# Performance work log

Measured on AMD Instinct MI355X. Metric: run time of the kernel, lower is better.

## Reference

```python
import jax, jax.numpy as jnp
import numpy as np

T, B, V, D, H, C = 2048, 32, 50257, 512, 768, 10


def setup_inputs() -> dict:
    key = jax.random.key(0)
    ks = jax.random.split(key, 11)
    s = 0.02
    return {
        "x": jax.random.randint(ks[0], (T, B), 0, V),
        "embed_table": jax.random.normal(ks[1], (V, D), jnp.float32) * s,
        "W_x": jax.random.normal(ks[2], (H, D), jnp.float32) * s,
        "W_f": jax.random.normal(ks[3], (H, D), jnp.float32) * s,
        "b_f": jax.random.normal(ks[4], (H,), jnp.float32) * s,
        "W_r": jax.random.normal(ks[5], (H, D), jnp.float32) * s,
        "b_r": jax.random.normal(ks[6], (H,), jnp.float32) * s,
        "W_cx": jax.random.normal(ks[7], (H, D), jnp.float32) * s,
        "b_cx": jax.random.normal(ks[8], (H,), jnp.float32) * s,
        "W_out": jax.random.normal(ks[9], (C, H), jnp.float32) * s,
        "b_out": jax.random.normal(ks[10], (C,), jnp.float32) * s,
    }


def reference(x, embed_table, W_x, W_f, b_f, W_r, b_r, W_cx, b_cx, W_out, b_out):
    # Embedding lookup: [T, B, D]
    e = embed_table[x]
    # Precompute all gate projections for every timestep (batched GEMMs).
    xp = jnp.einsum("tbd,hd->tbh", e, W_x)                 # x_t projection
    f = jax.nn.sigmoid(jnp.einsum("tbd,hd->tbh", e, W_f) + b_f)   # forget gate
    r = jax.nn.sigmoid(jnp.einsum("tbd,hd->tbh", e, W_r) + b_r)   # reset gate
    cx = jnp.einsum("tbd,hd->tbh", e, W_cx) + b_cx                # highway path

    c0 = jnp.zeros((B, H), e.dtype)  # init_hidden: zeros

    def step(c, inp):
        f_t, xp_t, r_t, cx_t = inp
        c = f_t * c + (1.0 - f_t) * xp_t
        h = r_t * jnp.tanh(c) + (1.0 - r_t) * cx_t
        return c, h

    _, ht = jax.lax.scan(step, c0, (f, xp, r, cx))  # ht: [T, B, H]

    # tanh -> max-pool over time -> tanh -> classifier
    pooled = jnp.max(jnp.tanh(ht), axis=0)          # [B, H]
    pooled = jnp.tanh(pooled)
    logit = pooled @ W_out.T + b_out                # [B, C]
    return logit
```

## Files before the change

### kernel.cpp

```cpp
#include <hip/hip_runtime.h>
#include <hip/hip_bf16.h>
#include <cstdint>
#include <cstddef>

#define T_DIM 2048
#define B_DIM 32
#define D_DIM 512
#define H_DIM 768
#define C_DIM 10
#define K_DIM D_DIM
#define N_DIM (4 * H_DIM)

#define TC 1024
#define NCHUNK (T_DIM / TC)
#define MC (TC * B_DIM)

#define L_SEG 64
#define S_SEG (TC / L_SEG)
#define BH (B_DIM * H_DIM)

typedef __attribute__((ext_vector_type(8))) short short8;
typedef __attribute__((ext_vector_type(4))) float float4v;

__device__ inline unsigned short f2bf(float f) {
  unsigned int u = __builtin_bit_cast(unsigned int, f);
  unsigned int r = (u + 0x7FFFu + ((u >> 16) & 1u)) >> 16;
  return (unsigned short)r;
}
__device__ inline float bf2f(unsigned short s) {
  unsigned int u = ((unsigned int)s) << 16;
  return __builtin_bit_cast(float, u);
}
__device__ inline float fast_rcp(float x) { return __builtin_amdgcn_rcpf(x); }
__device__ inline float fast_exp2(float x) { return __builtin_amdgcn_exp2f(x); }
__device__ inline float sigmoid_f(float x) {
  float e = fast_exp2(-1.4426950408889634f * x);
  return fast_rcp(1.0f + e);
}
__device__ inline float tanh_f(float x) {
  float e = fast_exp2(2.885390081777927f * x);
  return 1.0f - 2.0f * fast_rcp(e + 1.0f);
}
__device__ inline void gld16(const unsigned short* g, unsigned short* l) {
  __builtin_amdgcn_global_load_lds(
      (const __attribute__((address_space(1))) void*)g,
      (__attribute__((address_space(3))) void*)l, 16, 0, 0);
}
__device__ inline unsigned int pack_bf16x2(float lo, float hi) {
  return ((unsigned int)f2bf(hi) << 16) | (unsigned int)f2bf(lo);
}

__global__ __launch_bounds__(256) void gather_embed_kernel(
    const int* __restrict__ x_c, const float* __restrict__ table,
    unsigned short* __restrict__ ebfc) {
  int idx = blockIdx.x * 256 + threadIdx.x;
  int m = idx >> 7;
  int k4 = (idx & 127) << 2;
  int row = x_c[m];
  float4 v = *(const float4*)(table + (size_t)row * D_DIM + k4);
  ushort4 o;
  o.x = f2bf(v.x); o.y = f2bf(v.y); o.z = f2bf(v.z); o.w = f2bf(v.w);
  *(ushort4*)(ebfc + (size_t)m * D_DIM + k4) = o;
}

__global__ __launch_bounds__(256) void convert_w_kernel(
    const float* __restrict__ Wx, const float* __restrict__ Wf,
    const float* __restrict__ Wr, const float* __restrict__ Wcx,
    unsigned short* __restrict__ wcat) {
  int idx = blockIdx.x * 256 + threadIdx.x;
  int n = idx >> 7;
  int k4 = (idx & 127) << 2;
  int mat = n / H_DIM;
  int h = n - mat * H_DIM;
  const float* src = (mat == 0) ? Wx : (mat == 1) ? Wf : (mat == 2) ? Wr : Wcx;
  float4 v = *(const float4*)(src + (size_t)h * D_DIM + k4);
  ushort4 o;
  o.x = f2bf(v.x); o.y = f2bf(v.y); o.z = f2bf(v.z); o.w = f2bf(v.w);
  *(ushort4*)(wcat + (size_t)n * D_DIM + k4) = o;
}

#define BM 128
#define BN 128
#define BK 32

__global__ __launch_bounds__(256) void gemm_kernel(
    const unsigned short* __restrict__ ebfc,
    const unsigned short* __restrict__ wcat,
    const float* __restrict__ b_f, const float* __restrict__ b_r,
    const float* __restrict__ b_cx,
    unsigned short* __restrict__ projc) {
  __shared__ __align__(16) unsigned short As[2][4096];
  __shared__ __align__(16) unsigned short Bs[2][4096];

  int tid  = threadIdx.x;
  int wave = tid >> 6;
  int lane = tid & 63;
  int quad = lane >> 4;
  int l16  = lane & 15;
  int m0 = blockIdx.y * BM;
  int n0 = blockIdx.x * BN;
  int wn = (wave & 1) * 64;
  int wm = (wave >> 1) * 64;

  int row0 = tid >> 2;
  int cl0  = (tid & 3) ^ ((row0 >> 1) & 3);
  int row1 = 64 + row0;
  int cl1  = (tid & 3) ^ ((row1 >> 1) & 3);

  const unsigned short* gA0 = ebfc + (size_t)(m0 + row0) * K_DIM + cl0 * 8;
  const unsigned short* gA1 = ebfc + (size_t)(m0 + row1) * K_DIM + cl1 * 8;
  const unsigned short* gB0 = wcat + (size_t)(n0 + row0) * K_DIM + cl0 * 8;
  const unsigned short* gB1 = wcat + (size_t)(n0 + row1) * K_DIM + cl1 * 8;

  float4v acc[4][4] = {};

#define STAGE(buf, kt) do { \
    gld16(gA0 + (kt), As[buf] + tid * 8); \
    gld16(gB0 + (kt), Bs[buf] + tid * 8); \
    gld16(gA1 + (kt), As[buf] + 2048 + tid * 8); \
    gld16(gB1 + (kt), Bs[buf] + 2048 + tid * 8); } while (0)

  STAGE(0, 0);
  __syncthreads();

#pragma unroll
  for (int ki = 0; ki < K_DIM / BK; ki++) {
    const int cur = ki & 1;
    if (ki + 1 < K_DIM / BK) STAGE(cur ^ 1, (ki + 1) * BK);
    short8 wf[4], ef[4];
#pragma unroll
    for (int i = 0; i < 4; i++) {
      int r = wn + i * 16 + l16;
      int p = quad ^ ((r >> 1) & 3);
      wf[i] = *(const short8*)(Bs[cur] + r * BK + p * 8);
    }
#pragma unroll
    for (int j = 0; j < 4; j++) {
      int r = wm + j * 16 + l16;
      int p = quad ^ ((r >> 1) & 3);
      ef[j] = *(const short8*)(As[cur] + r * BK + p * 8);
    }
#pragma unroll
    for (int i = 0; i < 4; i++)
#pragma unroll
      for (int j = 0; j < 4; j++)
        acc[i][j] = __builtin_amdgcn_mfma_f32_16x16x32_bf16(wf[i], ef[j], acc[i][j], 0, 0, 0);
    __syncthreads();
  }

  int mat = n0 / H_DIM;
  int hb = n0 - mat * H_DIM;
  size_t matBase = (size_t)mat * MC * H_DIM;
  const float* bias = (mat == 1) ? b_f : (mat == 2) ? b_r : b_cx;
#pragma unroll
  for (int i = 0; i < 4; i++) {
    int h0 = hb + wn + i * 16 + quad * 4;
    float4 bv;
    if (mat == 0) { bv.x = bv.y = bv.z = bv.w = 0.0f; }
    else          { bv = *(const float4*)(bias + h0); }
#pragma unroll
    for (int j = 0; j < 4; j++) {
      int m = m0 + wm + j * 16 + l16;
      float v0 = acc[i][j][0] + bv.x;
      float v1 = acc[i][j][1] + bv.y;
      float v2 = acc[i][j][2] + bv.z;
      float v3 = acc[i][j][3] + bv.w;
      if (mat == 1 || mat == 2) {
        v0 = sigmoid_f(v0); v1 = sigmoid_f(v1);
        v2 = sigmoid_f(v2); v3 = sigmoid_f(v3);
      }
      uint2 pk;
      pk.x = pack_bf16x2(v0, v1);
      pk.y = pack_bf16x2(v2, v3);
      *(uint2*)(projc + matBase + (size_t)m * H_DIM + h0) = pk;
    }
  }
}

__global__ __launch_bounds__(128) void scan1_kernel(
    const unsigned short* __restrict__ projc,
    float* __restrict__ Pw, float* __restrict__ Qw) {
  int blk = blockIdx.x;
  int seg = blk / (BH / 512);
  int q   = blk % (BH / 512);
  int e4  = (q * 128 + threadIdx.x) * 4;
  const size_t mstr = (size_t)MC * H_DIM;
  size_t idx0 = (size_t)(seg * L_SEG) * BH + e4;
  float p0 = 1.f, p1 = 1.f, p2 = 1.f, p3 = 1.f;
  float c0 = 0.f, c1 = 0.f, c2 = 0.f, c3 = 0.f;
#pragma unroll 4
  for (int t = 0; t < L_SEG; t++) {
    size_t id = idx0 + (size_t)t * BH;
    ushort4 xp = *(const ushort4*)(projc + id);
    ushort4 ff = *(const ushort4*)(projc + mstr + id);
    float f0 = bf2f(ff.x), f1 = bf2f(ff.y), f2 = bf2f(ff.z), f3 = bf2f(ff.w);
    c0 = fmaf(f0, c0 - bf2f(xp.x), bf2f(xp.x));
    c1 = fmaf(f1, c1 - bf2f(xp.y), bf2f(xp.y));
    c2 = fmaf(f2, c2 - bf2f(xp.z), bf2f(xp.z));
    c3 = fmaf(f3, c3 - bf2f(xp.w), bf2f(xp.w));
    p0 *= f0; p1 *= f1; p2 *= f2; p3 *= f3;
  }
  int o = seg * BH + e4;
  *(float4*)(Pw + o) = make_float4(p0, p1, p2, p3);
  *(float4*)(Qw + o) = make_float4(c0, c1, c2, c3);
}

__global__ __launch_bounds__(256) void prefix_kernel(
    const float* __restrict__ Pw, const float* __restrict__ Qw,
    float* __restrict__ cin, float* __restrict__ c_state,
    const float* __restrict__ segmax, float* __restrict__ hm_state,
    int first, int hm_init) {
  int gid = blockIdx.x * 256 + threadIdx.x;
  float c = first ? 0.f : c_state[gid];
#pragma unroll
  for (int s = 0; s < S_SEG; s++) {
    cin[s * BH + gid] = c;
    c = fmaf(Pw[s * BH + gid], c, Qw[s * BH + gid]);
  }
  c_state[gid] = c;
  if (!first) {
    float m = segmax[gid];
#pragma unroll
    for (int s = 1; s < S_SEG; s++) m = fmaxf(m, segmax[s * BH + gid]);
    hm_state[gid] = hm_init ? m : fmaxf(hm_state[gid], m);
  }
}

__global__ __launch_bounds__(128) void scan2_kernel(
    const unsigned short* __restrict__ projc,
    const float* __restrict__ cin, float* __restrict__ segmax) {
  int blk = blockIdx.x;
  int seg = blk / (BH / 512);
  int q   = blk % (BH / 512);
  int e4  = (q * 128 + threadIdx.x) * 4;
  const size_t mstr = (size_t)MC * H_DIM;
  size_t idx0 = (size_t)(seg * L_SEG) * BH + e4;
  int o = seg * BH + e4;
  float4 cv = *(const float4*)(cin + o);
  float c0 = cv.x, c1 = cv.y, c2 = cv.z, c3 = cv.w;
  float m0 = -1e30f, m1 = -1e30f, m2 = -1e30f, m3 = -1e30f;
#pragma unroll 2
  for (int t = 0; t < L_SEG; t++) {
    size_t id = idx0 + (size_t)t * BH;
    ushort4 xp = *(const ushort4*)(projc + id);
    ushort4 ff = *(const ushort4*)(projc + mstr + id);
    ushort4 rr = *(const ushort4*)(projc + 2 * mstr + id);
    ushort4 cx = *(const ushort4*)(projc + 3 * mstr + id);
    c0 = fmaf(bf2f(ff.x), c0 - bf2f(xp.x), bf2f(xp.x));
    c1 = fmaf(bf2f(ff.y), c1 - bf2f(xp.y), bf2f(xp.y));
    c2 = fmaf(bf2f(ff.z), c2 - bf2f(xp.z), bf2f(xp.z));
    c3 = fmaf(bf2f(ff.w), c3 - bf2f(xp.w), bf2f(xp.w));
    float h0 = fmaf(bf2f(rr.x), tanh_f(c0) - bf2f(cx.x), bf2f(cx.x));
    float h1 = fmaf(bf2f(rr.y), tanh_f(c1) - bf2f(cx.y), bf2f(cx.y));
    float h2 = fmaf(bf2f(rr.z), tanh_f(c2) - bf2f(cx.z), bf2f(cx.z));
    float h3 = fmaf(bf2f(rr.w), tanh_f(c3) - bf2f(cx.w), bf2f(cx.w));
    m0 = fmaxf(m0, h0); m1 = fmaxf(m1, h1);
    m2 = fmaxf(m2, h2); m3 = fmaxf(m3, h3);
  }
  *(float4*)(segmax + o) = make_float4(m0, m1, m2, m3);
}

__global__ __launch_bounds__(256) void pool_final_kernel(
    const float* __restrict__ segmax, const float* __restrict__ hm_state,
    float* __restrict__ pooled) {
  int gid = blockIdx.x * 256 + threadIdx.x;
  float m = hm_state[gid];
#pragma unroll
  for (int s = 0; s < S_SEG; s++) m = fmaxf(m, segmax[s * BH + gid]);
  pooled[gid] = tanh_f(tanh_f(m));
}

__global__ __launch_bounds__(64) void classifier_kernel(
    const float* __restrict__ pooled, const float* __restrict__ W_out,
    const float* __restrict__ b_out, float* __restrict__ out) {
  int b = blockIdx.x / C_DIM;
  int c = blockIdx.x % C_DIM;
  int lane = threadIdx.x;
  float s = 0.0f;
#pragma unroll
  for (int i = 0; i < H_DIM / 64; i++) {
    int h = i * 64 + lane;
    s += pooled[(size_t)b * H_DIM + h] * W_out[(size_t)c * H_DIM + h];
  }
#pragma unroll
  for (int off = 32; off; off >>= 1) s += __shfl_down(s, off, 64);
  if (lane == 0) out[b * C_DIM + c] = s + b_out[c];
}

extern "C" void kernel_launch(void* const* d_in, const int* in_sizes, int n_in,
                              void* d_out, int out_size, void* d_ws, size_t ws_size,
                              hipStream_t stream) {
  const int*   x     = (const int*)d_in[0];
  const float* table = (const float*)d_in[1];
  const float* W_x   = (const float*)d_in[2];
  const float* W_f   = (const float*)d_in[3];
  const float* b_f   = (const float*)d_in[4];
  const float* W_r   = (const float*)d_in[5];
  const float* b_r   = (const float*)d_in[6];
  const float* W_cx  = (const float*)d_in[7];
  const float* b_cx  = (const float*)d_in[8];
  const float* W_out = (const float*)d_in[9];
  const float* b_out = (const float*)d_in[10];

  char* ws = (char*)d_ws;
  size_t off = 0;
  unsigned short* wcat  = (unsigned short*)(ws + off); off += (size_t)N_DIM * K_DIM * 2;
  unsigned short* ebfc  = (unsigned short*)(ws + off); off += (size_t)MC * K_DIM * 2;
  unsigned short* projc = (unsigned short*)(ws + off); off += (size_t)4 * MC * H_DIM * 2;
  float* Pw     = (float*)(ws + off); off += (size_t)S_SEG * BH * 4;
  float* Qw     = (float*)(ws + off); off += (size_t)S_SEG * BH * 4;
  float* cin    = (float*)(ws + off); off += (size_t)S_SEG * BH * 4;
  float* segmax = (float*)(ws + off); off += (size_t)S_SEG * BH * 4;
  float* c_st   = (float*)(ws + off); off += (size_t)BH * 4;
  float* hm_st  = (float*)(ws + off); off += (size_t)BH * 4;
  float* pooled = (float*)(ws + off); off += (size_t)BH * 4;

  convert_w_kernel<<<(N_DIM * K_DIM / 4) / 256, 256, 0, stream>>>(W_x, W_f, W_r, W_cx, wcat);

  dim3 g(N_DIM / BN, MC / BM);
  for (int ch = 0; ch < NCHUNK; ch++) {
    gather_embed_kernel<<<(MC * K_DIM / 4) / 256, 256, 0, stream>>>(x + (size_t)ch * MC, table, ebfc);
    gemm_kernel<<<g, 256, 0, stream>>>(ebfc, wcat, b_f, b_r, b_cx, projc);
    scan1_kernel<<<S_SEG * (BH / 512), 128, 0, stream>>>(projc, Pw, Qw);
    prefix_kernel<<<BH / 256, 256, 0, stream>>>(Pw, Qw, cin, c_st, segmax, hm_st,
                                                ch == 0, ch == 1);
    scan2_kernel<<<S_SEG * (BH / 512), 128, 0, stream>>>(projc, cin, segmax);
  }
  pool_final_kernel<<<BH / 256, 256, 0, stream>>>(segmax, hm_st, pooled);
  classifier_kernel<<<B_DIM * C_DIM, 64, 0, stream>>>(pooled, W_out, b_out, (float*)d_out);
}
```

Measured before the change: 610.2 us.

## Load GEMM MFMA fragments directly from global memory into registers, drop LDS staging

The projection GEMM no longer stages A/B tiles through shared memory with global_load_lds and barriers. Each wave loads its own MFMA fragments straight from global memory into double-buffered registers, prefetching the next K slice. The launch bounds also request three blocks per CU. This removes the LDS traffic and the __syncthreads calls, but loses the sharing of tiles across waves, so each element is fetched from global/L2 twice as often, and the extra register buffers may add register pressure.

```diff
diff --git a/kernel.cpp b/kernel.cpp
--- a/kernel.cpp
+++ b/kernel.cpp
@@ -40,11 +40,6 @@
 __device__ inline float tanh_f(float x) {
   float e = fast_exp2(2.885390081777927f * x);
   return 1.0f - 2.0f * fast_rcp(e + 1.0f);
-}
-__device__ inline void gld16(const unsigned short* g, unsigned short* l) {
-  __builtin_amdgcn_global_load_lds(
-      (const __attribute__((address_space(1))) void*)g,
-      (__attribute__((address_space(3))) void*)l, 16, 0, 0);
 }
 __device__ inline unsigned int pack_bf16x2(float lo, float hi) {
   return ((unsigned int)f2bf(hi) << 16) | (unsigned int)f2bf(lo);
@@ -83,15 +78,12 @@
 #define BN 128
 #define BK 32
 
-__global__ __launch_bounds__(256) void gemm_kernel(
+__global__ __launch_bounds__(256, 3) void gemm_kernel(
     const unsigned short* __restrict__ ebfc,
     const unsigned short* __restrict__ wcat,
     const float* __restrict__ b_f, const float* __restrict__ b_r,
     const float* __restrict__ b_cx,
     unsigned short* __restrict__ projc) {
-  __shared__ __align__(16) unsigned short As[2][4096];
-  __shared__ __align__(16) unsigned short Bs[2][4096];
-
   int tid  = threadIdx.x;
   int wave = tid >> 6;
   int lane = tid & 63;
@@ -102,50 +94,39 @@
   int wn = (wave & 1) * 64;
   int wm = (wave >> 1) * 64;
 
-  int row0 = tid >> 2;
-  int cl0  = (tid & 3) ^ ((row0 >> 1) & 3);
-  int row1 = 64 + row0;
-  int cl1  = (tid & 3) ^ ((row1 >> 1) & 3);
-
-  const unsigned short* gA0 = ebfc + (size_t)(m0 + row0) * K_DIM + cl0 * 8;
-  const unsigned short* gA1 = ebfc + (size_t)(m0 + row1) * K_DIM + cl1 * 8;
-  const unsigned short* gB0 = wcat + (size_t)(n0 + row0) * K_DIM + cl0 * 8;
-  const unsigned short* gB1 = wcat + (size_t)(n0 + row1) * K_DIM + cl1 * 8;
+  const unsigned short* aw[4];
+  const unsigned short* ae[4];
+#pragma unroll
+  for (int i = 0; i < 4; i++)
+    aw[i] = wcat + (size_t)(n0 + wn + i * 16 + l16) * K_DIM + quad * 8;
+#pragma unroll
+  for (int j = 0; j < 4; j++)
+    ae[j] = ebfc + (size_t)(m0 + wm + j * 16 + l16) * K_DIM + quad * 8;
 
   float4v acc[4][4] = {};
-
-#define STAGE(buf, kt) do { \
-    gld16(gA0 + (kt), As[buf] + tid * 8); \
-    gld16(gB0 + (kt), Bs[buf] + tid * 8); \
-    gld16(gA1 + (kt), As[buf] + 2048 + tid * 8); \
-    gld16(gB1 + (kt), Bs[buf] + 2048 + tid * 8); } while (0)
-
-  STAGE(0, 0);
-  __syncthreads();
+  short8 wf[2][4], ef[2][4];
+#pragma unroll
+  for (int i = 0; i < 4; i++) {
+    wf[0][i] = *(const short8*)(aw[i]);
+    ef[0][i] = *(const short8*)(ae[i]);
+  }
 
 #pragma unroll
   for (int ki = 0; ki < K_DIM / BK; ki++) {
-    const int cur = ki & 1;
-    if (ki + 1 < K_DIM / BK) STAGE(cur ^ 1, (ki + 1) * BK);
-    short8 wf[4], ef[4];
-#pragma unroll
-    for (int i = 0; i < 4; i++) {
-      int r = wn + i * 16 + l16;
-      int p = quad ^ ((r >> 1) & 3);
-      wf[i] = *(const short8*)(Bs[cur] + r * BK + p * 8);
+    const int cur = ki & 1, nxt = cur ^ 1;
+    if (ki + 1 < K_DIM / BK) {
+      const int ko = (ki + 1) * BK;
+#pragma unroll
+      for (int i = 0; i < 4; i++) {
+        wf[nxt][i] = *(const short8*)(aw[i] + ko);
+        ef[nxt][i] = *(const short8*)(ae[i] + ko);
+      }
     }
 #pragma unroll
-    for (int j = 0; j < 4; j++) {
-      int r = wm + j * 16 + l16;
-      int p = quad ^ ((r >> 1) & 3);
-      ef[j] = *(const short8*)(As[cur] + r * BK + p * 8);
-    }
-#pragma unroll
     for (int i = 0; i < 4; i++)
 #pragma unroll
       for (int j = 0; j < 4; j++)
-        acc[i][j] = __builtin_amdgcn_mfma_f32_16x16x32_bf16(wf[i], ef[j], acc[i][j], 0, 0, 0);
-    __syncthreads();
+        acc[i][j] = __builtin_amdgcn_mfma_f32_16x16x32_bf16(wf[cur][i], ef[cur][j], acc[i][j], 0, 0, 0);
   }
 
   int mat = n0 / H_DIM;
```

After: 1.045 ms. 1.71x slower.
